# Optimization experiments

Hardware: AMD Instinct MI355X
Metric: run time of the kernel (lower is better)

Reference implementation:

```python
import jax, jax.numpy as jnp
import numpy as np

B, NL, C, H, W = 4, 2048, 128, 128, 128
N_PTS0, N_PTS1 = 32, 8
SCALE = N_PTS0 // N_PTS1  # MaxPool1d kernel/stride
FEATURE_DIM = 5
BN_EPS = 1e-5


def setup_inputs() -> dict:
    key = jax.random.key(0)
    ks = jax.random.split(key, 12)
    fm = jax.random.normal(ks[0], (B, C, H, W), dtype=jnp.float32)
    lines = jax.random.uniform(ks[1], (B, NL, 2, 2), dtype=jnp.float32) * 128.0
    P = C // 2
    s = 0.05
    return {
        "feature_map": fm,
        "lines": lines,
        # Bottleneck1D params (BatchNorm in eval mode: running_mean=0, running_var=1)
        "bn1_g": jnp.ones((C,), jnp.float32), "bn1_b": jnp.zeros((C,), jnp.float32),
        "conv1_w": jax.random.normal(ks[2], (P, C, 1), jnp.float32) * s,
        "conv1_b": jnp.zeros((P,), jnp.float32),
        "bn2_g": jnp.ones((P,), jnp.float32), "bn2_b": jnp.zeros((P,), jnp.float32),
        "conv2_w": jax.random.normal(ks[3], (P, P, 3), jnp.float32) * s,
        "conv2_b": jnp.zeros((P,), jnp.float32),
        "bn3_g": jnp.ones((P,), jnp.float32), "bn3_b": jnp.zeros((P,), jnp.float32),
        "conv3_w": jax.random.normal(ks[4], (C, P, 1), jnp.float32) * s,
        "conv3_b": jnp.zeros((C,), jnp.float32),
        # fc2: ReLU -> Linear(dim_loi*n_pts1 + 5, 4)
        "fc2_w": jax.random.normal(ks[5], (4, C * N_PTS1 + FEATURE_DIM), jnp.float32) * s,
        "fc2_b": jnp.zeros((4,), jnp.float32),
    }


def _bn(x, g, b):
    # eval-mode BatchNorm1d with running_mean=0, running_var=1
    return x * (g / jnp.sqrt(1.0 + BN_EPS))[None, :, None] + b[None, :, None]


def _conv1d(x, w, b, pad):
    y = jax.lax.conv_general_dilated(x, w, (1,), [(pad, pad)],
                                     dimension_numbers=("NCH", "OIH", "NCH"))
    return y + b[None, :, None]


def _loi_gather(fm, lines):
    # sample points along each line: [B, NL, N_PTS0, 2]
    lam = jnp.linspace(0.0, 1.0, N_PTS0, dtype=jnp.float32)[None, None, :, None]
    p = lines[:, :, 0:1, :] * lam + lines[:, :, 1:2, :] * (1.0 - lam) - 0.5
    p = p.reshape(B, -1, 2)                      # [B, NL*N_PTS0, 2]
    px, py = p[..., 0], p[..., 1]
    px0 = jnp.clip(jnp.floor(px), 0.0, 127.0)
    py0 = jnp.clip(jnp.floor(py), 0.0, 127.0)
    px1 = jnp.clip(px0 + 1.0, 0.0, 127.0)
    py1 = jnp.clip(py0 + 1.0, 0.0, 127.0)
    px0l, py0l = px0.astype(jnp.int32), py0.astype(jnp.int32)
    px1l, py1l = px1.astype(jnp.int32), py1.astype(jnp.int32)

    gather = jax.vmap(lambda f, yi, xi: f[:, yi, xi])  # [C, P] per image
    # weights exactly as in the torch source
    xp = (gather(fm, py0l, px0l) * ((px1 - px) * (py1 - py))[:, None, :]
          + gather(fm, py1l, px0l) * ((px - px0) * (py1 - py))[:, None, :]
          + gather(fm, py0l, px1l) * ((px1 - px) * (py - py0))[:, None, :]
          + gather(fm, py1l, px1l) * ((px - px0) * (py - py0))[:, None, :])
    # [B, C, NL*N_PTS0] -> [B*NL, C, N_PTS0]
    xp = xp.reshape(B, C, NL, N_PTS0).transpose(0, 2, 1, 3).reshape(B * NL, C, N_PTS0)
    return xp


def reference(feature_map, lines, bn1_g, bn1_b, conv1_w, conv1_b,
              bn2_g, bn2_b, conv2_w, conv2_b, bn3_g, bn3_b,
              conv3_w, conv3_b, fc2_w, fc2_b):
    xp = _loi_gather(feature_map, lines)               # [B*NL, C, N_PTS0]
    # MaxPool1d(SCALE, SCALE)
    x = xp.reshape(B * NL, C, N_PTS1, SCALE).max(axis=-1)
    # Bottleneck1D residual block
    y = jax.nn.relu(_bn(x, bn1_g, bn1_b))
    y = _conv1d(y, conv1_w, conv1_b, 0)
    y = jax.nn.relu(_bn(y, bn2_g, bn2_b))
    y = _conv1d(y, conv2_w, conv2_b, 1)
    y = jax.nn.relu(_bn(y, bn3_g, bn3_b))
    y = _conv1d(y, conv3_w, conv3_b, 0)
    x = x + y                                          # [B*NL, C, N_PTS1]
    # line geometry feature (use_cood=1, use_slop=1)
    xyu, xyv = lines[:, :, 0, :], lines[:, :, 1, :]
    u2v = jnp.sqrt(((xyu - xyv) ** 2).sum(-1, keepdims=True)).clip(min=1e-6)
    f = jnp.concatenate([xyu / 128.0, xyv / 128.0, u2v], axis=-1)
    f = f.reshape(B * NL, FEATURE_DIM)
    # concat + fc2 (ReLU -> Linear)
    x = jnp.concatenate([x.reshape(B * NL, C * N_PTS1), f], axis=1)
    logits = jax.nn.relu(x) @ fc2_w.T + fc2_b
    prob = jax.nn.softmax(logits, axis=1)
    return logits, prob
```

## Files before the change

kernel.cpp:

```cpp
#include <hip/hip_runtime.h>
#include <math.h>

#define BB 4
#define NLL 2048
#define CC 128
#define HH 128
#define WW 128
#define NPTS0 32
#define NPTS1 8
#define PP 64
#define FDIM 5
#define FCK (CC*NPTS1 + FDIM)
#define FCKP 1032

typedef __attribute__((ext_vector_type(8))) short bf16x8;
typedef __attribute__((ext_vector_type(4))) float f32x4;
typedef __attribute__((ext_vector_type(2))) float f32x2;
typedef __attribute__((ext_vector_type(4))) unsigned u32x4;

__device__ __forceinline__ unsigned short f2bf(float f) {
    union { float f; unsigned u; } v; v.f = f;
    unsigned u = v.u;
    return (unsigned short)((u + 0x7fffu + ((u >> 16) & 1u)) >> 16);
}
__device__ __forceinline__ float bf2f(unsigned short s) {
    union { unsigned u; float f; } v; v.u = ((unsigned)s) << 16;
    return v.f;
}
__device__ __forceinline__ unsigned cvt_pk_bf16(float a, float b) {
    unsigned r;
    asm("v_cvt_pk_bf16_f32 %0, %1, %2" : "=v"(r) : "v"(a), "v"(b));
    return r;
}
__device__ __forceinline__ f32x2 pk_mul(f32x2 a, f32x2 b) {
    f32x2 d;
    asm("v_pk_mul_f32 %0, %1, %2" : "=v"(d) : "v"(a), "v"(b));
    return d;
}
__device__ __forceinline__ f32x2 pk_fma(f32x2 a, f32x2 b, f32x2 c) {
    f32x2 d;
    asm("v_pk_fma_f32 %0, %1, %2, %3" : "=v"(d) : "v"(a), "v"(b), "v"(c));
    return d;
}
__device__ __forceinline__ f32x2 bfpair(unsigned u) {
    union { unsigned v; float f; } lo, hi;
    lo.v = u << 16;
    hi.v = u & 0xffff0000u;
    f32x2 r; r.x = lo.f; r.y = hi.f;
    return r;
}

__global__ __launch_bounds__(256)
void transpose_prep(const float* __restrict__ fm, const float* __restrict__ w1,
                    const float* __restrict__ w2, const float* __restrict__ w3,
                    const float* __restrict__ fcw,
                    unsigned short* __restrict__ fmT,
                    unsigned short* __restrict__ W1b,
                    unsigned short* __restrict__ W2b,
                    unsigned short* __restrict__ W3b,
                    float* __restrict__ fcwP) {
    const int t = threadIdx.x;
    if (blockIdx.x >= 2048) {
        int gid = (blockIdx.x - 2048) * 256 + t;
        for (int e = gid; e < 32800; e += 4096) {
            if (e < 8192) {
                W1b[e] = f2bf(w1[e]);
            } else if (e < 20480) {
                int g = e - 8192;
                int tt = g >> 12, r = g & 4095;
                int p = r >> 6, q = r & 63;
                W2b[tt * 4096 + p * 64 + q] = f2bf(w2[p * 192 + q * 3 + tt]);
            } else if (e < 28672) {
                int g = e - 20480;
                W3b[g] = f2bf(w3[g]);
            } else {
                int g = e - 28672;
                int o = g / FCKP, r = g - o * FCKP;
                fcwP[g] = (r < FCK) ? fcw[o * FCK + r] : 0.0f;
            }
        }
        return;
    }
    __shared__ unsigned short tile[64 * 72];
    const int bh = blockIdx.x;
    const int by = bh >> 2;
    const int xh = (bh >> 1) & 1;
    const int ch = bh & 1;
    const int b = by >> 7, y = by & 127;
    const float* src = fm + ((size_t)b * CC + ch * 64) * (HH * WW)
                     + (size_t)y * WW + xh * 64;
    const int x4 = (t & 15) * 4;
    #pragma unroll
    for (int i = 0; i < 4; ++i) {
        int r = (t >> 4) + 16 * i;
        float4 v = *(const float4*)&src[(size_t)r * (HH * WW) + x4];
        uint2 u;
        u.x = cvt_pk_bf16(v.x, v.y);
        u.y = cvt_pk_bf16(v.z, v.w);
        *(uint2*)&tile[r * 72 + (x4 ^ (r & 28))] = u;
    }
    __syncthreads();
    const int c4 = (t & 15) * 4;
    unsigned short* dst = fmT + ((size_t)by * WW + xh * 64) * CC + ch * 64;
    #pragma unroll
    for (int i = 0; i < 4; ++i) {
        int x = (t >> 4) + 16 * i;
        ushort4 u;
        u.x = tile[(c4 + 0) * 72 + (x ^ ((c4 + 0) & 28))];
        u.y = tile[(c4 + 1) * 72 + (x ^ ((c4 + 1) & 28))];
        u.z = tile[(c4 + 2) * 72 + (x ^ ((c4 + 2) & 28))];
        u.w = tile[(c4 + 3) * 72 + (x ^ ((c4 + 3) & 28))];
        *(ushort4*)&dst[(size_t)x * CC + c4] = u;
    }
}

__global__ __launch_bounds__(256, 5)
void line_mfma(const unsigned short* __restrict__ fmT,
               const float* __restrict__ lines,
               const float* __restrict__ bn1_g, const float* __restrict__ bn1_b,
               const unsigned short* __restrict__ W1b, const float* __restrict__ b1,
               const float* __restrict__ bn2_g, const float* __restrict__ bn2_b,
               const unsigned short* __restrict__ W2b, const float* __restrict__ b2,
               const float* __restrict__ bn3_g, const float* __restrict__ bn3_b,
               const unsigned short* __restrict__ W3b, const float* __restrict__ b3,
               const float* __restrict__ fcwP,  const float* __restrict__ fcb,
               float* __restrict__ out) {
    __shared__ int   s_oA[64], s_oB[64], s_oC[64], s_oD[64];
    __shared__ float s_wA[64], s_wB[64], s_wC[64], s_wD[64];
    __shared__ float s_xs[16 * 132];
    __shared__ unsigned short s_ybn[16 * 136];
    __shared__ unsigned short s_z1[2 * 10 * 72];
    __shared__ unsigned short s_z2[16 * 72];
    __shared__ float s_feat[2][8];
    __shared__ float s_red[4 * 8];

    const int bx  = blockIdx.x;
    const int wg  = (bx & 7) * 512 + (bx >> 3);
    const int L0  = wg * 2;
    const int b   = wg >> 10;
    const int tid = threadIdx.x;
    const int lane = tid & 63;
    const int wv   = tid >> 6;
    const int quad = lane >> 4;
    const int l16  = lane & 15;
    const float inv_s = 1.0f / sqrtf(1.0f + 1e-5f);

    if (tid < 64) {
        int line = tid >> 5, pt = tid & 31;
        const float* ln = lines + (size_t)(L0 + line) * 4;
        float lam = (float)pt * (1.0f / 31.0f);
        float om  = 1.0f - lam;
        float px = ln[0] * lam + ln[2] * om - 0.5f;
        float py = ln[1] * lam + ln[3] * om - 0.5f;
        float px0 = fminf(fmaxf(floorf(px), 0.0f), 127.0f);
        float py0 = fminf(fmaxf(floorf(py), 0.0f), 127.0f);
        float px1 = fminf(px0 + 1.0f, 127.0f);
        float py1 = fminf(py0 + 1.0f, 127.0f);
        int ix0 = (int)px0, ix1 = (int)px1, iy0 = (int)py0, iy1 = (int)py1;
        s_oA[tid] = (iy0 * WW + ix0) * CC;
        s_oB[tid] = (iy1 * WW + ix0) * CC;
        s_oC[tid] = (iy0 * WW + ix1) * CC;
        s_oD[tid] = (iy1 * WW + ix1) * CC;
        float ax = px1 - px, bxv = px - px0, ay = py1 - py, byv = py - py0;
        s_wA[tid] = ax  * ay;
        s_wB[tid] = bxv * ay;
        s_wC[tid] = ax  * byv;
        s_wD[tid] = bxv * byv;
    }
    if (tid >= 64 && tid < 66) {
        int line = tid - 64;
        const float* ln = lines + (size_t)(L0 + line) * 4;
        float ux = ln[0], uy = ln[1], vx = ln[2], vy = ln[3];
        float dx = ux - vx, dy = uy - vy;
        float d = fmaxf(sqrtf(dx * dx + dy * dy), 1e-6f);
        s_feat[line][0] = ux * (1.0f / 128.0f);
        s_feat[line][1] = uy * (1.0f / 128.0f);
        s_feat[line][2] = vx * (1.0f / 128.0f);
        s_feat[line][3] = vy * (1.0f / 128.0f);
        s_feat[line][4] = d;
    }
    if (tid < 128) {
        int line = tid >> 6, q = tid & 63;
        s_z1[line * 720 + 0 * 72 + q] = 0;
        s_z1[line * 720 + 9 * 72 + q] = 0;
    }
    __syncthreads();

    {
        int tl = tid >> 4;
        int c8 = (tid & 15) * 8;
        const unsigned short* base = fmT + (size_t)b * (HH * WW * CC) + c8;
        const int pt0 = (tl >> 3) * 32 + (tl & 7) * 4;
        u32x4 rA[4], rB[4], rC[4], rD[4];
        #pragma unroll
        for (int j = 0; j < 4; ++j) {
            rA[j] = *(const u32x4*)(base + s_oA[pt0 + j]);
            rB[j] = *(const u32x4*)(base + s_oB[pt0 + j]);
            rC[j] = *(const u32x4*)(base + s_oC[pt0 + j]);
            rD[j] = *(const u32x4*)(base + s_oD[pt0 + j]);
        }
        float acc[8];
        #pragma unroll
        for (int i = 0; i < 8; ++i) acc[i] = -INFINITY;
        #pragma unroll
        for (int j = 0; j < 4; ++j) {
            int pt = pt0 + j;
            float wA = s_wA[pt], wB = s_wB[pt], wC = s_wC[pt], wD = s_wD[pt];
            f32x2 wA2 = {wA, wA}, wB2 = {wB, wB};
            f32x2 wC2 = {wC, wC}, wD2 = {wD, wD};
            #pragma unroll
            for (int p2 = 0; p2 < 4; ++p2) {
                f32x2 t = pk_mul(wA2, bfpair(rA[j][p2]));
                t = pk_fma(wB2, bfpair(rB[j][p2]), t);
                t = pk_fma(wC2, bfpair(rC[j][p2]), t);
                t = pk_fma(wD2, bfpair(rD[j][p2]), t);
                acc[2 * p2]     = fmaxf(acc[2 * p2],     t.x);
                acc[2 * p2 + 1] = fmaxf(acc[2 * p2 + 1], t.y);
            }
        }
        float* xr = &s_xs[tl * 132 + c8];
        f32x4 lo = {acc[0], acc[1], acc[2], acc[3]};
        f32x4 hi = {acc[4], acc[5], acc[6], acc[7]};
        *(f32x4*)&xr[0] = lo;
        *(f32x4*)&xr[4] = hi;
        float4 g0 = *(const float4*)(bn1_g + c8);
        float4 g1 = *(const float4*)(bn1_g + c8 + 4);
        float4 v0 = *(const float4*)(bn1_b + c8);
        float4 v1 = *(const float4*)(bn1_b + c8 + 4);
        float y0 = fmaxf(acc[0] * (g0.x * inv_s) + v0.x, 0.0f);
        float y1 = fmaxf(acc[1] * (g0.y * inv_s) + v0.y, 0.0f);
        float y2 = fmaxf(acc[2] * (g0.z * inv_s) + v0.z, 0.0f);
        float y3 = fmaxf(acc[3] * (g0.w * inv_s) + v0.w, 0.0f);
        float y4 = fmaxf(acc[4] * (g1.x * inv_s) + v1.x, 0.0f);
        float y5 = fmaxf(acc[5] * (g1.y * inv_s) + v1.y, 0.0f);
        float y6 = fmaxf(acc[6] * (g1.z * inv_s) + v1.z, 0.0f);
        float y7 = fmaxf(acc[7] * (g1.w * inv_s) + v1.w, 0.0f);
        u32x4 pk;
        pk[0] = cvt_pk_bf16(y0, y1);
        pk[1] = cvt_pk_bf16(y2, y3);
        pk[2] = cvt_pk_bf16(y4, y5);
        pk[3] = cvt_pk_bf16(y6, y7);
        *(u32x4*)&s_ybn[tl * 136 + c8] = pk;
    }
    __syncthreads();

    {
        int n0 = wv * 16;
        f32x4 acc = {0.f, 0.f, 0.f, 0.f};
        #pragma unroll
        for (int kc = 0; kc < 4; ++kc) {
            bf16x8 a = *(const bf16x8*)&s_ybn[l16 * 136 + kc * 32 + quad * 8];
            bf16x8 bf = *(const bf16x8*)(W1b + (n0 + l16) * 128 + kc * 32 + quad * 8);
            acc = __builtin_amdgcn_mfma_f32_16x16x32_bf16(a, bf, acc, 0, 0, 0);
        }
        int p = n0 + l16;
        float s2 = bn2_g[p] * inv_s, bb2 = bn2_b[p], cb = b1[p];
        int line = quad >> 1;
        int kbase = (quad & 1) * 4;
        float v0 = fmaxf((acc[0] + cb) * s2 + bb2, 0.0f);
        float v1 = fmaxf((acc[1] + cb) * s2 + bb2, 0.0f);
        float v2 = fmaxf((acc[2] + cb) * s2 + bb2, 0.0f);
        float v3 = fmaxf((acc[3] + cb) * s2 + bb2, 0.0f);
        unsigned pk01 = cvt_pk_bf16(v0, v1);
        unsigned pk23 = cvt_pk_bf16(v2, v3);
        unsigned short* zr = &s_z1[line * 720 + (kbase + 1) * 72 + p];
        zr[0 * 72] = (unsigned short)pk01;
        zr[1 * 72] = (unsigned short)(pk01 >> 16);
        zr[2 * 72] = (unsigned short)pk23;
        zr[3 * 72] = (unsigned short)(pk23 >> 16);
    }
    __syncthreads();

    {
        int n0 = wv * 16;
        f32x4 acc = {0.f, 0.f, 0.f, 0.f};
        int line = l16 >> 3, k = l16 & 7;
        #pragma unroll
        for (int t = 0; t < 3; ++t) {
            const unsigned short* arow = &s_z1[line * 720 + (k + t) * 72];
            #pragma unroll
            for (int kc = 0; kc < 2; ++kc) {
                bf16x8 a = *(const bf16x8*)&arow[kc * 32 + quad * 8];
                bf16x8 bf = *(const bf16x8*)(W2b + t * 4096 + (n0 + l16) * 64 + kc * 32 + quad * 8);
                acc = __builtin_amdgcn_mfma_f32_16x16x32_bf16(a, bf, acc, 0, 0, 0);
            }
        }
        int p = n0 + l16;
        float s3 = bn3_g[p] * inv_s, bb3 = bn3_b[p], cb = b2[p];
        float v0 = fmaxf((acc[0] + cb) * s3 + bb3, 0.0f);
        float v1 = fmaxf((acc[1] + cb) * s3 + bb3, 0.0f);
        float v2 = fmaxf((acc[2] + cb) * s3 + bb3, 0.0f);
        float v3 = fmaxf((acc[3] + cb) * s3 + bb3, 0.0f);
        unsigned pk01 = cvt_pk_bf16(v0, v1);
        unsigned pk23 = cvt_pk_bf16(v2, v3);
        unsigned short* zr = &s_z2[(quad * 4) * 72 + p];
        zr[0 * 72] = (unsigned short)pk01;
        zr[1 * 72] = (unsigned short)(pk01 >> 16);
        zr[2 * 72] = (unsigned short)pk23;
        zr[3 * 72] = (unsigned short)(pk23 >> 16);
    }
    __syncthreads();

    f32x2 P0 = {0.f, 0.f}, P1v = {0.f, 0.f}, P2v = {0.f, 0.f}, P3v = {0.f, 0.f};
    {
        int kbase = (quad & 1) * 4;
        bf16x8 a0 = *(const bf16x8*)&s_z2[l16 * 72 + 0 * 32 + quad * 8];
        bf16x8 a1 = *(const bf16x8*)&s_z2[l16 * 72 + 1 * 32 + quad * 8];
        #pragma unroll
        for (int sub = 0; sub < 2; ++sub) {
            int n0 = wv * 32 + sub * 16;
            f32x4 acc = {0.f, 0.f, 0.f, 0.f};
            bf16x8 bf0 = *(const bf16x8*)(W3b + (n0 + l16) * 64 + 0 * 32 + quad * 8);
            bf16x8 bf1 = *(const bf16x8*)(W3b + (n0 + l16) * 64 + 1 * 32 + quad * 8);
            acc = __builtin_amdgcn_mfma_f32_16x16x32_bf16(a0, bf0, acc, 0, 0, 0);
            acc = __builtin_amdgcn_mfma_f32_16x16x32_bf16(a1, bf1, acc, 0, 0, 0);
            int c = n0 + l16;
            float cb = b3[c];
            int idx = c * 8 + kbase;
            float4 w0 = *(const float4*)(fcwP + 0 * FCKP + idx);
            float4 w1w = *(const float4*)(fcwP + 1 * FCKP + idx);
            float4 w2w = *(const float4*)(fcwP + 2 * FCKP + idx);
            float4 w3w = *(const float4*)(fcwP + 3 * FCKP + idx);
            #pragma unroll
            for (int rp = 0; rp < 2; ++rp) {
                int m = quad * 4 + rp * 2;
                float e0 = fmaxf(s_xs[m * 132 + c] + acc[rp * 2] + cb, 0.0f);
                float e1 = fmaxf(s_xs[(m + 1) * 132 + c] + acc[rp * 2 + 1] + cb, 0.0f);
                f32x2 vv = {e0, e1};
                float w0lo = rp ? w0.z : w0.x,  w0hi = rp ? w0.w : w0.y;
                float w1lo = rp ? w1w.z : w1w.x, w1hi = rp ? w1w.w : w1w.y;
                float w2lo = rp ? w2w.z : w2w.x, w2hi = rp ? w2w.w : w2w.y;
                float w3lo = rp ? w3w.z : w3w.x, w3hi = rp ? w3w.w : w3w.y;
                f32x2 w0p = {w0lo, w0hi}, w1p = {w1lo, w1hi};
                f32x2 w2p = {w2lo, w2hi}, w3p = {w3lo, w3hi};
                P0  = pk_fma(vv, w0p, P0);
                P1v = pk_fma(vv, w1p, P1v);
                P2v = pk_fma(vv, w2p, P2v);
                P3v = pk_fma(vv, w3p, P3v);
            }
        }
    }
    float p0 = P0.x + P0.y, p1 = P1v.x + P1v.y;
    float p2 = P2v.x + P2v.y, p3 = P3v.x + P3v.y;
    #pragma unroll
    for (int off = 16; off >= 1; off >>= 1) {
        p0 += __shfl_down(p0, off);
        p1 += __shfl_down(p1, off);
        p2 += __shfl_down(p2, off);
        p3 += __shfl_down(p3, off);
    }
    if ((lane & 31) == 0) {
        int line = lane >> 5;
        s_red[wv * 8 + line * 4 + 0] = p0;
        s_red[wv * 8 + line * 4 + 1] = p1;
        s_red[wv * 8 + line * 4 + 2] = p2;
        s_red[wv * 8 + line * 4 + 3] = p3;
    }
    __syncthreads();

    if (tid < 2) {
        int line = tid;
        float lg[4];
        #pragma unroll
        for (int o = 0; o < 4; ++o) {
            lg[o] = fcb[o] + s_red[0 + line * 4 + o] + s_red[8 + line * 4 + o]
                  + s_red[16 + line * 4 + o] + s_red[24 + line * 4 + o];
        }
        #pragma unroll
        for (int j = 0; j < FDIM; ++j) {
            float fv = fmaxf(s_feat[line][j], 0.0f);
            #pragma unroll
            for (int o = 0; o < 4; ++o)
                lg[o] = fmaf(fv, fcwP[o * FCKP + 1024 + j], lg[o]);
        }
        float m = fmaxf(fmaxf(lg[0], lg[1]), fmaxf(lg[2], lg[3]));
        float e0 = expf(lg[0] - m), e1 = expf(lg[1] - m);
        float e2 = expf(lg[2] - m), e3 = expf(lg[3] - m);
        float inv = 1.0f / (e0 + e1 + e2 + e3);
        float* lo = out + (size_t)(L0 + line) * 4;
        lo[0] = lg[0]; lo[1] = lg[1]; lo[2] = lg[2]; lo[3] = lg[3];
        float* pr = out + (size_t)BB * NLL * 4 + (size_t)(L0 + line) * 4;
        pr[0] = e0 * inv; pr[1] = e1 * inv; pr[2] = e2 * inv; pr[3] = e3 * inv;
    }
}

__global__ __launch_bounds__(256)
void transpose_fm2(const float* __restrict__ fm, float* __restrict__ fmT) {
    __shared__ float tile[32 * 132];
    const int c0 = blockIdx.x * 32;
    const int by = blockIdx.y;
    const int b = by >> 7, y = by & 127;
    const int t = threadIdx.x;
    const float* src = fm + ((size_t)b * CC) * (HH * WW) + (size_t)y * WW;
    const int x4 = (t & 31) * 4;
    #pragma unroll
    for (int i = 0; i < 4; ++i) {
        int r = (t >> 5) + 8 * i;
        *(float4*)&tile[r * 132 + x4] =
            *(const float4*)&src[(size_t)(c0 + r) * (HH * WW) + x4];
    }
    __syncthreads();
    float* dst = fmT + (size_t)by * WW * CC + c0 + (t & 31);
    const int cr = (t & 31) * 132;
    #pragma unroll
    for (int i = 0; i < 16; ++i) {
        int x = (t >> 5) + 8 * i;
        dst[(size_t)x * CC] = tile[cr + x];
    }
}

template<bool TRANS>
__global__ __launch_bounds__(256)
void line_kernel_v1(const float* __restrict__ fm,
                    const float* __restrict__ lines,
                    const float* __restrict__ bn1_g, const float* __restrict__ bn1_b,
                    const float* __restrict__ w1,    const float* __restrict__ b1,
                    const float* __restrict__ bn2_g, const float* __restrict__ bn2_b,
                    const float* __restrict__ w2,    const float* __restrict__ b2,
                    const float* __restrict__ bn3_g, const float* __restrict__ bn3_b,
                    const float* __restrict__ w3,    const float* __restrict__ b3,
                    const float* __restrict__ fcw,   const float* __restrict__ fcb,
                    float* __restrict__ out) {
    __shared__ int   s_ix0[32], s_ix1[32], s_iy0[32], s_iy1[32];
    __shared__ float s_wA[32], s_wB[32], s_wC[32], s_wD[32];
    __shared__ float xs [8][132];
    __shared__ float ybn[8][132];
    __shared__ float z1 [64][12];
    __shared__ float z2 [64][8];
    __shared__ float s_feat[8];
    __shared__ float s_red[16];

    const int L   = blockIdx.x;
    const int b   = L / NLL;
    const int tid = threadIdx.x;
    const float inv_s = 1.0f / sqrtf(1.0f + 1e-5f);
    const float* ln = lines + (size_t)L * 4;

    if (tid < 32) {
        float lam = (float)tid * (1.0f / 31.0f);
        float om  = 1.0f - lam;
        float px = ln[0] * lam + ln[2] * om - 0.5f;
        float py = ln[1] * lam + ln[3] * om - 0.5f;
        float px0 = fminf(fmaxf(floorf(px), 0.0f), 127.0f);
        float py0 = fminf(fmaxf(floorf(py), 0.0f), 127.0f);
        float px1 = fminf(px0 + 1.0f, 127.0f);
        float py1 = fminf(py0 + 1.0f, 127.0f);
        s_ix0[tid] = (int)px0; s_ix1[tid] = (int)px1;
        s_iy0[tid] = (int)py0; s_iy1[tid] = (int)py1;
        float ax = px1 - px, bxv = px - px0, ay = py1 - py, byv = py - py0;
        s_wA[tid] = ax  * ay;  s_wB[tid] = bxv * ay;
        s_wC[tid] = ax  * byv; s_wD[tid] = bxv * byv;
    }
    if (tid == 0) {
        float ux = ln[0], uy = ln[1], vx = ln[2], vy = ln[3];
        float dx = ux - vx, dy = uy - vy;
        float d = fmaxf(sqrtf(dx * dx + dy * dy), 1e-6f);
        s_feat[0] = ux / 128.0f; s_feat[1] = uy / 128.0f;
        s_feat[2] = vx / 128.0f; s_feat[3] = vy / 128.0f;
        s_feat[4] = d;
    }
    __syncthreads();
    {
        int cq = tid & 31, k = tid >> 5, c0 = cq * 4;
        float4 acc;
        acc.x = -INFINITY; acc.y = -INFINITY; acc.z = -INFINITY; acc.w = -INFINITY;
        #pragma unroll
        for (int j = 0; j < 4; ++j) {
            int pt = k * 4 + j;
            int ix0 = s_ix0[pt], ix1 = s_ix1[pt];
            int iy0 = s_iy0[pt], iy1 = s_iy1[pt];
            float wA = s_wA[pt], wB = s_wB[pt], wC = s_wC[pt], wD = s_wD[pt];
            float4 vA, vB, vC, vD;
            if (TRANS) {
                const float* base = fm + (size_t)b * HH * WW * CC;
                vA = *(const float4*)(base + ((size_t)(iy0 * WW + ix0)) * CC + c0);
                vB = *(const float4*)(base + ((size_t)(iy1 * WW + ix0)) * CC + c0);
                vC = *(const float4*)(base + ((size_t)(iy0 * WW + ix1)) * CC + c0);
                vD = *(const float4*)(base + ((size_t)(iy1 * WW + ix1)) * CC + c0);
            } else {
                const float* base = fm + ((size_t)b * CC + c0) * HH * WW;
                int oA = iy0 * WW + ix0, oB = iy1 * WW + ix0;
                int oC = iy0 * WW + ix1, oD = iy1 * WW + ix1;
                vA.x = base[oA];           vB.x = base[oB];
                vC.x = base[oC];           vD.x = base[oD];
                vA.y = base[HH*WW + oA];   vB.y = base[HH*WW + oB];
                vC.y = base[HH*WW + oC];   vD.y = base[HH*WW + oD];
                vA.z = base[2*HH*WW + oA]; vB.z = base[2*HH*WW + oB];
                vC.z = base[2*HH*WW + oC]; vD.z = base[2*HH*WW + oD];
                vA.w = base[3*HH*WW + oA]; vB.w = base[3*HH*WW + oB];
                vC.w = base[3*HH*WW + oC]; vD.w = base[3*HH*WW + oD];
            }
            float4 v;
            v.x = wA * vA.x + wB * vB.x + wC * vC.x + wD * vD.x;
            v.y = wA * vA.y + wB * vB.y + wC * vC.y + wD * vD.y;
            v.z = wA * vA.z + wB * vB.z + wC * vC.z + wD * vD.z;
            v.w = wA * vA.w + wB * vB.w + wC * vC.w + wD * vD.w;
            acc.x = fmaxf(acc.x, v.x); acc.y = fmaxf(acc.y, v.y);
            acc.z = fmaxf(acc.z, v.z); acc.w = fmaxf(acc.w, v.w);
        }
        *(float4*)(&xs[k][c0]) = acc;
    }
    __syncthreads();
    for (int e = tid; e < 1024; e += 256) {
        int k = e >> 7, c = e & 127;
        ybn[k][c] = fmaxf(xs[k][c] * (bn1_g[c] * inv_s) + bn1_b[c], 0.0f);
    }
    __syncthreads();
    if (tid < 64) { z1[tid][0] = 0.0f; z1[tid][9] = 0.0f; }
    {
        int p = tid >> 2, kq = tid & 3;
        const float* wrow = w1 + p * 128;
        float a0a = 0.f, a0b = 0.f, a1a = 0.f, a1b = 0.f;
        #pragma unroll 8
        for (int c = 0; c < 128; c += 4) {
            float4 w  = *(const float4*)(wrow + c);
            float4 ya = *(const float4*)(&ybn[kq][c]);
            float4 yb = *(const float4*)(&ybn[kq + 4][c]);
            a0a = fmaf(w.x, ya.x, a0a); a0b = fmaf(w.y, ya.y, a0b);
            a0a = fmaf(w.z, ya.z, a0a); a0b = fmaf(w.w, ya.w, a0b);
            a1a = fmaf(w.x, yb.x, a1a); a1b = fmaf(w.y, yb.y, a1b);
            a1a = fmaf(w.z, yb.z, a1a); a1b = fmaf(w.w, yb.w, a1b);
        }
        float s2 = bn2_g[p] * inv_s, bb = bn2_b[p], cb = b1[p];
        z1[p][1 + kq]     = fmaxf((a0a + a0b + cb) * s2 + bb, 0.0f);
        z1[p][1 + kq + 4] = fmaxf((a1a + a1b + cb) * s2 + bb, 0.0f);
    }
    __syncthreads();
    {
        int p = tid >> 2, kq = tid & 3;
        const float* wrow = w2 + p * 192;
        float acc0 = 0.f, acc1 = 0.f;
        #pragma unroll 4
        for (int q = 0; q < 64; ++q) {
            float w0 = wrow[q * 3 + 0], w1v = wrow[q * 3 + 1], w2v = wrow[q * 3 + 2];
            const float* zr = &z1[q][0];
            acc0 = fmaf(w0, zr[kq], acc0);
            acc0 = fmaf(w1v, zr[kq + 1], acc0);
            acc0 = fmaf(w2v, zr[kq + 2], acc0);
            acc1 = fmaf(w0, zr[kq + 4], acc1);
            acc1 = fmaf(w1v, zr[kq + 5], acc1);
            acc1 = fmaf(w2v, zr[kq + 6], acc1);
        }
        float s3 = bn3_g[p] * inv_s, bb = bn3_b[p], cb = b2[p];
        z2[p][kq]     = fmaxf((acc0 + cb) * s3 + bb, 0.0f);
        z2[p][kq + 4] = fmaxf((acc1 + cb) * s3 + bb, 0.0f);
    }
    __syncthreads();
    float part0 = 0.f, part1 = 0.f, part2 = 0.f, part3 = 0.f;
    {
        int c = tid >> 1, kq = tid & 1;
        const float* wrow = w3 + c * 64;
        float acc[4] = {0.f, 0.f, 0.f, 0.f};
        #pragma unroll 8
        for (int q = 0; q < 64; ++q) {
            float w = wrow[q];
            acc[0] = fmaf(w, z2[q][kq], acc[0]);
            acc[1] = fmaf(w, z2[q][kq + 2], acc[1]);
            acc[2] = fmaf(w, z2[q][kq + 4], acc[2]);
            acc[3] = fmaf(w, z2[q][kq + 6], acc[3]);
        }
        float cb = b3[c];
        #pragma unroll
        for (int i = 0; i < 4; ++i) {
            int k = kq + 2 * i;
            float v = fmaxf(xs[k][c] + acc[i] + cb, 0.0f);
            int idx = c * 8 + k;
            part0 = fmaf(v, fcw[0 * FCK + idx], part0);
            part1 = fmaf(v, fcw[1 * FCK + idx], part1);
            part2 = fmaf(v, fcw[2 * FCK + idx], part2);
            part3 = fmaf(v, fcw[3 * FCK + idx], part3);
        }
    }
    #pragma unroll
    for (int off = 32; off > 0; off >>= 1) {
        part0 += __shfl_down(part0, off);
        part1 += __shfl_down(part1, off);
        part2 += __shfl_down(part2, off);
        part3 += __shfl_down(part3, off);
    }
    if ((tid & 63) == 0) {
        int w = tid >> 6;
        s_red[w * 4 + 0] = part0; s_red[w * 4 + 1] = part1;
        s_red[w * 4 + 2] = part2; s_red[w * 4 + 3] = part3;
    }
    __syncthreads();
    if (tid == 0) {
        float lg[4];
        #pragma unroll
        for (int o = 0; o < 4; ++o)
            lg[o] = fcb[o] + s_red[o] + s_red[4 + o] + s_red[8 + o] + s_red[12 + o];
        #pragma unroll
        for (int j = 0; j < FDIM; ++j) {
            float fv = fmaxf(s_feat[j], 0.0f);
            #pragma unroll
            for (int o = 0; o < 4; ++o)
                lg[o] = fmaf(fv, fcw[o * FCK + 1024 + j], lg[o]);
        }
        float m = fmaxf(fmaxf(lg[0], lg[1]), fmaxf(lg[2], lg[3]));
        float e0 = expf(lg[0] - m), e1 = expf(lg[1] - m);
        float e2 = expf(lg[2] - m), e3 = expf(lg[3] - m);
        float inv = 1.0f / (e0 + e1 + e2 + e3);
        float* lo = out + (size_t)L * 4;
        lo[0] = lg[0]; lo[1] = lg[1]; lo[2] = lg[2]; lo[3] = lg[3];
        float* pr = out + (size_t)BB * NLL * 4 + (size_t)L * 4;
        pr[0] = e0 * inv; pr[1] = e1 * inv; pr[2] = e2 * inv; pr[3] = e3 * inv;
    }
}

extern "C" void kernel_launch(void* const* d_in, const int* in_sizes, int n_in,
                              void* d_out, int out_size, void* d_ws, size_t ws_size,
                              hipStream_t stream) {
    const float* fm     = (const float*)d_in[0];
    const float* lines  = (const float*)d_in[1];
    const float* bn1_g  = (const float*)d_in[2];
    const float* bn1_b  = (const float*)d_in[3];
    const float* w1     = (const float*)d_in[4];
    const float* b1     = (const float*)d_in[5];
    const float* bn2_g  = (const float*)d_in[6];
    const float* bn2_b  = (const float*)d_in[7];
    const float* w2     = (const float*)d_in[8];
    const float* b2     = (const float*)d_in[9];
    const float* bn3_g  = (const float*)d_in[10];
    const float* bn3_b  = (const float*)d_in[11];
    const float* w3     = (const float*)d_in[12];
    const float* b3     = (const float*)d_in[13];
    const float* fcw    = (const float*)d_in[14];
    const float* fcb    = (const float*)d_in[15];
    float* out = (float*)d_out;

    const size_t fmTb_bytes = (size_t)BB * HH * WW * CC * sizeof(unsigned short);
    const size_t fmTf_bytes = (size_t)BB * HH * WW * CC * sizeof(float);
    const size_t wb_bytes   = 57344;
    const size_t fcwP_bytes = 4 * FCKP * sizeof(float);

    if (ws_size >= fmTb_bytes + wb_bytes + fcwP_bytes) {
        unsigned short* fmT = (unsigned short*)d_ws;
        unsigned short* W1b = (unsigned short*)((char*)d_ws + fmTb_bytes);
        unsigned short* W2b = W1b + 8192;
        unsigned short* W3b = W2b + 12288;
        float* fcwP = (float*)((char*)d_ws + fmTb_bytes + wb_bytes);
        transpose_prep<<<2048 + 16, 256, 0, stream>>>(
            fm, w1, w2, w3, fcw, fmT, W1b, W2b, W3b, fcwP);
        line_mfma<<<BB * NLL / 2, 256, 0, stream>>>(
            fmT, lines, bn1_g, bn1_b, W1b, b1, bn2_g, bn2_b, W2b, b2,
            bn3_g, bn3_b, W3b, b3, fcwP, fcb, out);
    } else if (ws_size >= fmTf_bytes) {
        float* fmT = (float*)d_ws;
        dim3 tg(CC / 32, BB * HH);
        transpose_fm2<<<tg, 256, 0, stream>>>(fm, fmT);
        line_kernel_v1<true><<<BB * NLL, 256, 0, stream>>>(
            fmT, lines, bn1_g, bn1_b, w1, b1, bn2_g, bn2_b, w2, b2,
            bn3_g, bn3_b, w3, b3, fcw, fcb, out);
    } else {
        line_kernel_v1<false><<<BB * NLL, 256, 0, stream>>>(
            fm, lines, bn1_g, bn1_b, w1, b1, bn2_g, bn2_b, w2, b2,
            bn3_g, bn3_b, w3, b3, fcw, fcb, out);
    }
}
```

Measured before the change: 150.5 us.

## Process two line pairs per block and prefetch the second gather during the conv chain

Each block now handles four lines as two pairs instead of two lines. The bilinear gather loads for the second pair are issued before the first pair's MFMA conv chain and consumed afterwards, hiding global-gather latency behind compute. __syncthreads is replaced with an LDS-only waitcnt plus s_barrier so in-flight global loads are not drained at barriers. The cost is more live VGPRs, with the launch-bounds occupancy hint lowered from 5 to 4, and half as many blocks.

```diff
diff --git a/kernel.cpp b/kernel.cpp
--- a/kernel.cpp
+++ b/kernel.cpp
@@ -48,6 +48,10 @@
     hi.v = u & 0xffff0000u;
     f32x2 r; r.x = lo.f; r.y = hi.f;
     return r;
+}
+__device__ __forceinline__ void bar_lds() {
+    asm volatile("s_waitcnt lgkmcnt(0)" ::: "memory");
+    __builtin_amdgcn_s_barrier();
 }
 
 __global__ __launch_bounds__(256)
@@ -114,7 +118,7 @@
     }
 }
 
-__global__ __launch_bounds__(256, 5)
+__global__ __launch_bounds__(256, 4)
 void line_mfma(const unsigned short* __restrict__ fmT,
                const float* __restrict__ lines,
                const float* __restrict__ bn1_g, const float* __restrict__ bn1_b,
@@ -125,19 +129,19 @@
                const unsigned short* __restrict__ W3b, const float* __restrict__ b3,
                const float* __restrict__ fcwP,  const float* __restrict__ fcb,
                float* __restrict__ out) {
-    __shared__ int   s_oA[64], s_oB[64], s_oC[64], s_oD[64];
-    __shared__ float s_wA[64], s_wB[64], s_wC[64], s_wD[64];
+    __shared__ int   s_oA[128], s_oB[128], s_oC[128], s_oD[128];
+    __shared__ float s_wA[128], s_wB[128], s_wC[128], s_wD[128];
     __shared__ float s_xs[16 * 132];
     __shared__ unsigned short s_ybn[16 * 136];
     __shared__ unsigned short s_z1[2 * 10 * 72];
     __shared__ unsigned short s_z2[16 * 72];
-    __shared__ float s_feat[2][8];
+    __shared__ float s_feat[4][8];
     __shared__ float s_red[4 * 8];
 
     const int bx  = blockIdx.x;
-    const int wg  = (bx & 7) * 512 + (bx >> 3);
-    const int L0  = wg * 2;
-    const int b   = wg >> 10;
+    const int wg  = (bx & 7) * 256 + (bx >> 3);
+    const int L0  = wg * 4;
+    const int b   = wg >> 9;
     const int tid = threadIdx.x;
     const int lane = tid & 63;
     const int wv   = tid >> 6;
@@ -145,7 +149,7 @@
     const int l16  = lane & 15;
     const float inv_s = 1.0f / sqrtf(1.0f + 1e-5f);
 
-    if (tid < 64) {
+    if (tid < 128) {
         int line = tid >> 5, pt = tid & 31;
         const float* ln = lines + (size_t)(L0 + line) * 4;
         float lam = (float)pt * (1.0f / 31.0f);
@@ -167,8 +171,8 @@
         s_wC[tid] = ax  * byv;
         s_wD[tid] = bxv * byv;
     }
-    if (tid >= 64 && tid < 66) {
-        int line = tid - 64;
+    if (tid >= 128 && tid < 132) {
+        int line = tid - 128;
         const float* ln = lines + (size_t)(L0 + line) * 4;
         float ux = ln[0], uy = ln[1], vx = ln[2], vy = ln[3];
         float dx = ux - vx, dy = uy - vy;
@@ -179,32 +183,44 @@
         s_feat[line][3] = vy * (1.0f / 128.0f);
         s_feat[line][4] = d;
     }
-    if (tid < 128) {
-        int line = tid >> 6, q = tid & 63;
+    if (tid >= 132 && tid < 260 && tid - 132 < 128) {
+        int e = tid - 132;
+        int line = e >> 6, q = e & 63;
         s_z1[line * 720 + 0 * 72 + q] = 0;
         s_z1[line * 720 + 9 * 72 + q] = 0;
     }
-    __syncthreads();
-
-    {
-        int tl = tid >> 4;
-        int c8 = (tid & 15) * 8;
-        const unsigned short* base = fmT + (size_t)b * (HH * WW * CC) + c8;
-        const int pt0 = (tl >> 3) * 32 + (tl & 7) * 4;
-        u32x4 rA[4], rB[4], rC[4], rD[4];
+    if (tid < 4) {
+        int e = 124 + tid;
+        int line = e >> 6, q = e & 63;
+        s_z1[line * 720 + 0 * 72 + q] = 0;
+        s_z1[line * 720 + 9 * 72 + q] = 0;
+    }
+    bar_lds();
+
+    const int tl = tid >> 4;
+    const int c8 = (tid & 15) * 8;
+    const unsigned short* gbase = fmT + (size_t)b * (HH * WW * CC) + c8;
+
+    auto gather_issue = [&](int pair, u32x4* rA, u32x4* rB, u32x4* rC, u32x4* rD) {
+        int ptb = (pair * 2 + (tl >> 3)) * 32 + (tl & 7) * 4;
         #pragma unroll
         for (int j = 0; j < 4; ++j) {
-            rA[j] = *(const u32x4*)(base + s_oA[pt0 + j]);
-            rB[j] = *(const u32x4*)(base + s_oB[pt0 + j]);
-            rC[j] = *(const u32x4*)(base + s_oC[pt0 + j]);
-            rD[j] = *(const u32x4*)(base + s_oD[pt0 + j]);
-        }
+            rA[j] = *(const u32x4*)(gbase + s_oA[ptb + j]);
+            rB[j] = *(const u32x4*)(gbase + s_oB[ptb + j]);
+            rC[j] = *(const u32x4*)(gbase + s_oC[ptb + j]);
+            rD[j] = *(const u32x4*)(gbase + s_oD[ptb + j]);
+        }
+    };
+
+    auto bilinear = [&](int pair, const u32x4* rA, const u32x4* rB,
+                        const u32x4* rC, const u32x4* rD) {
+        int ptb = (pair * 2 + (tl >> 3)) * 32 + (tl & 7) * 4;
         float acc[8];
         #pragma unroll
         for (int i = 0; i < 8; ++i) acc[i] = -INFINITY;
         #pragma unroll
         for (int j = 0; j < 4; ++j) {
-            int pt = pt0 + j;
+            int pt = ptb + j;
             float wA = s_wA[pt], wB = s_wB[pt], wC = s_wC[pt], wD = s_wD[pt];
             f32x2 wA2 = {wA, wA}, wB2 = {wB, wB};
             f32x2 wC2 = {wC, wC}, wD2 = {wD, wD};
@@ -241,147 +257,168 @@
         pk[2] = cvt_pk_bf16(y4, y5);
         pk[3] = cvt_pk_bf16(y6, y7);
         *(u32x4*)&s_ybn[tl * 136 + c8] = pk;
-    }
-    __syncthreads();
+    };
+
+    auto conv_chain = [&]() {
+        {
+            int n0 = wv * 16;
+            f32x4 acc = {0.f, 0.f, 0.f, 0.f};
+            #pragma unroll
+            for (int kc = 0; kc < 4; ++kc) {
+                bf16x8 a = *(const bf16x8*)&s_ybn[l16 * 136 + kc * 32 + quad * 8];
+                bf16x8 bf = *(const bf16x8*)(W1b + (n0 + l16) * 128 + kc * 32 + quad * 8);
+                acc = __builtin_amdgcn_mfma_f32_16x16x32_bf16(a, bf, acc, 0, 0, 0);
+            }
+            int p = n0 + l16;
+            float s2 = bn2_g[p] * inv_s, bb2 = bn2_b[p], cb = b1[p];
+            int line = quad >> 1;
+            int kbase = (quad & 1) * 4;
+            float v0 = fmaxf((acc[0] + cb) * s2 + bb2, 0.0f);
+            float v1 = fmaxf((acc[1] + cb) * s2 + bb2, 0.0f);
+            float v2 = fmaxf((acc[2] + cb) * s2 + bb2, 0.0f);
+            float v3 = fmaxf((acc[3] + cb) * s2 + bb2, 0.0f);
+            unsigned pk01 = cvt_pk_bf16(v0, v1);
+            unsigned pk23 = cvt_pk_bf16(v2, v3);
+            unsigned short* zr = &s_z1[line * 720 + (kbase + 1) * 72 + p];
+            zr[0 * 72] = (unsigned short)pk01;
+            zr[1 * 72] = (unsigned short)(pk01 >> 16);
+            zr[2 * 72] = (unsigned short)pk23;
+            zr[3 * 72] = (unsigned short)(pk23 >> 16);
+        }
+        bar_lds();
+        {
+            int n0 = wv * 16;
+            f32x4 acc = {0.f, 0.f, 0.f, 0.f};
+            int line = l16 >> 3, k = l16 & 7;
+            #pragma unroll
+            for (int t = 0; t < 3; ++t) {
+                const unsigned short* arow = &s_z1[line * 720 + (k + t) * 72];
+                #pragma unroll
+                for (int kc = 0; kc < 2; ++kc) {
+                    bf16x8 a = *(const bf16x8*)&arow[kc * 32 + quad * 8];
+                    bf16x8 bf = *(const bf16x8*)(W2b + t * 4096 + (n0 + l16) * 64 + kc * 32 + quad * 8);
+                    acc = __builtin_amdgcn_mfma_f32_16x16x32_bf16(a, bf, acc, 0, 0, 0);
+                }
+            }
+            int p = n0 + l16;
+            float s3 = bn3_g[p] * inv_s, bb3 = bn3_b[p], cb = b2[p];
+            float v0 = fmaxf((acc[0] + cb) * s3 + bb3, 0.0f);
+            float v1 = fmaxf((acc[1] + cb) * s3 + bb3, 0.0f);
+            float v2 = fmaxf((acc[2] + cb) * s3 + bb3, 0.0f);
+            float v3 = fmaxf((acc[3] + cb) * s3 + bb3, 0.0f);
+            unsigned pk01 = cvt_pk_bf16(v0, v1);
+            unsigned pk23 = cvt_pk_bf16(v2, v3);
+            unsigned short* zr = &s_z2[(quad * 4) * 72 + p];
+            zr[0 * 72] = (unsigned short)pk01;
+            zr[1 * 72] = (unsigned short)(pk01 >> 16);
+            zr[2 * 72] = (unsigned short)pk23;
+            zr[3 * 72] = (unsigned short)(pk23 >> 16);
+        }
+        bar_lds();
+        f32x2 P0 = {0.f, 0.f}, P1v = {0.f, 0.f}, P2v = {0.f, 0.f}, P3v = {0.f, 0.f};
+        {
+            int kbase = (quad & 1) * 4;
+            bf16x8 a0 = *(const bf16x8*)&s_z2[l16 * 72 + 0 * 32 + quad * 8];
+            bf16x8 a1 = *(const bf16x8*)&s_z2[l16 * 72 + 1 * 32 + quad * 8];
+            #pragma unroll
+            for (int sub = 0; sub < 2; ++sub) {
+                int n0 = wv * 32 + sub * 16;
+                f32x4 acc = {0.f, 0.f, 0.f, 0.f};
+                bf16x8 bf0 = *(const bf16x8*)(W3b + (n0 + l16) * 64 + 0 * 32 + quad * 8);
+                bf16x8 bf1 = *(const bf16x8*)(W3b + (n0 + l16) * 64 + 1 * 32 + quad * 8);
+                acc = __builtin_amdgcn_mfma_f32_16x16x32_bf16(a0, bf0, acc, 0, 0, 0);
+                acc = __builtin_amdgcn_mfma_f32_16x16x32_bf16(a1, bf1, acc, 0, 0, 0);
+                int c = n0 + l16;
+                float cb = b3[c];
+                int idx = c * 8 + kbase;
+                float4 w0 = *(const float4*)(fcwP + 0 * FCKP + idx);
+                float4 w1w = *(const float4*)(fcwP + 1 * FCKP + idx);
+                float4 w2w = *(const float4*)(fcwP + 2 * FCKP + idx);
+                float4 w3w = *(const float4*)(fcwP + 3 * FCKP + idx);
+                #pragma unroll
+                for (int rp = 0; rp < 2; ++rp) {
+                    int m = quad * 4 + rp * 2;
+                    float e0 = fmaxf(s_xs[m * 132 + c] + acc[rp * 2] + cb, 0.0f);
+                    float e1 = fmaxf(s_xs[(m + 1) * 132 + c] + acc[rp * 2 + 1] + cb, 0.0f);
+                    f32x2 vv = {e0, e1};
+                    float w0lo = rp ? w0.z : w0.x,  w0hi = rp ? w0.w : w0.y;
+                    float w1lo = rp ? w1w.z : w1w.x, w1hi = rp ? w1w.w : w1w.y;
+                    float w2lo = rp ? w2w.z : w2w.x, w2hi = rp ? w2w.w : w2w.y;
+                    float w3lo = rp ? w3w.z : w3w.x, w3hi = rp ? w3w.w : w3w.y;
+                    f32x2 w0p = {w0lo, w0hi}, w1p = {w1lo, w1hi};
+                    f32x2 w2p = {w2lo, w2hi}, w3p = {w3lo, w3hi};
+                    P0  = pk_fma(vv, w0p, P0);
+                    P1v = pk_fma(vv, w1p, P1v);
+                    P2v = pk_fma(vv, w2p, P2v);
+                    P3v = pk_fma(vv, w3p, P3v);
+                }
+            }
+        }
+        float p0 = P0.x + P0.y, p1 = P1v.x + P1v.y;
+        float p2 = P2v.x + P2v.y, p3 = P3v.x + P3v.y;
+        #pragma unroll
+        for (int off = 16; off >= 1; off >>= 1) {
+            p0 += __shfl_down(p0, off);
+            p1 += __shfl_down(p1, off);
+            p2 += __shfl_down(p2, off);
+            p3 += __shfl_down(p3, off);
+        }
+        if ((lane & 31) == 0) {
+            int line = lane >> 5;
+            s_red[wv * 8 + line * 4 + 0] = p0;
+            s_red[wv * 8 + line * 4 + 1] = p1;
+            s_red[wv * 8 + line * 4 + 2] = p2;
+            s_red[wv * 8 + line * 4 + 3] = p3;
+        }
+        bar_lds();
+    };
+
+    auto finish = [&](int pair) {
+        if (tid < 2) {
+            int line = tid;
+            float lg[4];
+            #pragma unroll
+            for (int o = 0; o < 4; ++o) {
+                lg[o] = fcb[o] + s_red[0 + line * 4 + o] + s_red[8 + line * 4 + o]
+                      + s_red[16 + line * 4 + o] + s_red[24 + line * 4 + o];
+            }
+            #pragma unroll
+            for (int j = 0; j < FDIM; ++j) {
+                float fv = fmaxf(s_feat[pair * 2 + line][j], 0.0f);
+                #pragma unroll
+                for (int o = 0; o < 4; ++o)
+                    lg[o] = fmaf(fv, fcwP[o * FCKP + 1024 + j], lg[o]);
+            }
+            float m = fmaxf(fmaxf(lg[0], lg[1]), fmaxf(lg[2], lg[3]));
+            float e0 = expf(lg[0] - m), e1 = expf(lg[1] - m);
+            float e2 = expf(lg[2] - m), e3 = expf(lg[3] - m);
+            float inv = 1.0f / (e0 + e1 + e2 + e3);
+            size_t Lg = (size_t)(L0 + pair * 2 + line);
+            float* lo = out + Lg * 4;
+            lo[0] = lg[0]; lo[1] = lg[1]; lo[2] = lg[2]; lo[3] = lg[3];
+            float* pr = out + (size_t)BB * NLL * 4 + Lg * 4;
+            pr[0] = e0 * inv; pr[1] = e1 * inv; pr[2] = e2 * inv; pr[3] = e3 * inv;
+        }
+    };
 
     {
-        int n0 = wv * 16;
-        f32x4 acc = {0.f, 0.f, 0.f, 0.f};
-        #pragma unroll
-        for (int kc = 0; kc < 4; ++kc) {
-            bf16x8 a = *(const bf16x8*)&s_ybn[l16 * 136 + kc * 32 + quad * 8];
-            bf16x8 bf = *(const bf16x8*)(W1b + (n0 + l16) * 128 + kc * 32 + quad * 8);
-            acc = __builtin_amdgcn_mfma_f32_16x16x32_bf16(a, bf, acc, 0, 0, 0);
-        }
-        int p = n0 + l16;
-        float s2 = bn2_g[p] * inv_s, bb2 = bn2_b[p], cb = b1[p];
-        int line = quad >> 1;
-        int kbase = (quad & 1) * 4;
-        float v0 = fmaxf((acc[0] + cb) * s2 + bb2, 0.0f);
-        float v1 = fmaxf((acc[1] + cb) * s2 + bb2, 0.0f);
-        float v2 = fmaxf((acc[2] + cb) * s2 + bb2, 0.0f);
-        float v3 = fmaxf((acc[3] + cb) * s2 + bb2, 0.0f);
-        unsigned pk01 = cvt_pk_bf16(v0, v1);
-        unsigned pk23 = cvt_pk_bf16(v2, v3);
-        unsigned short* zr = &s_z1[line * 720 + (kbase + 1) * 72 + p];
-        zr[0 * 72] = (unsigned short)pk01;
-        zr[1 * 72] = (unsigned short)(pk01 >> 16);
-        zr[2 * 72] = (unsigned short)pk23;
-        zr[3 * 72] = (unsigned short)(pk23 >> 16);
-    }
-    __syncthreads();
-
-    {
-        int n0 = wv * 16;
-        f32x4 acc = {0.f, 0.f, 0.f, 0.f};
-        int line = l16 >> 3, k = l16 & 7;
-        #pragma unroll
-        for (int t = 0; t < 3; ++t) {
-            const unsigned short* arow = &s_z1[line * 720 + (k + t) * 72];
-            #pragma unroll
-            for (int kc = 0; kc < 2; ++kc) {
-                bf16x8 a = *(const bf16x8*)&arow[kc * 32 + quad * 8];
-                bf16x8 bf = *(const bf16x8*)(W2b + t * 4096 + (n0 + l16) * 64 + kc * 32 + quad * 8);
-                acc = __builtin_amdgcn_mfma_f32_16x16x32_bf16(a, bf, acc, 0, 0, 0);
-            }
-        }
-        int p = n0 + l16;
-        float s3 = bn3_g[p] * inv_s, bb3 = bn3_b[p], cb = b2[p];
-        float v0 = fmaxf((acc[0] + cb) * s3 + bb3, 0.0f);
-        float v1 = fmaxf((acc[1] + cb) * s3 + bb3, 0.0f);
-        float v2 = fmaxf((acc[2] + cb) * s3 + bb3, 0.0f);
-        float v3 = fmaxf((acc[3] + cb) * s3 + bb3, 0.0f);
-        unsigned pk01 = cvt_pk_bf16(v0, v1);
-        unsigned pk23 = cvt_pk_bf16(v2, v3);
-        unsigned short* zr = &s_z2[(quad * 4) * 72 + p];
-        zr[0 * 72] = (unsigned short)pk01;
-        zr[1 * 72] = (unsigned short)(pk01 >> 16);
-        zr[2 * 72] = (unsigned short)pk23;
-        zr[3 * 72] = (unsigned short)(pk23 >> 16);
-    }
-    __syncthreads();
-
-    f32x2 P0 = {0.f, 0.f}, P1v = {0.f, 0.f}, P2v = {0.f, 0.f}, P3v = {0.f, 0.f};
-    {
-        int kbase = (quad & 1) * 4;
-        bf16x8 a0 = *(const bf16x8*)&s_z2[l16 * 72 + 0 * 32 + quad * 8];
-        bf16x8 a1 = *(const bf16x8*)&s_z2[l16 * 72 + 1 * 32 + quad * 8];
-        #pragma unroll
-        for (int sub = 0; sub < 2; ++sub) {
-            int n0 = wv * 32 + sub * 16;
-            f32x4 acc = {0.f, 0.f, 0.f, 0.f};
-            bf16x8 bf0 = *(const bf16x8*)(W3b + (n0 + l16) * 64 + 0 * 32 + quad * 8);
-            bf16x8 bf1 = *(const bf16x8*)(W3b + (n0 + l16) * 64 + 1 * 32 + quad * 8);
-            acc = __builtin_amdgcn_mfma_f32_16x16x32_bf16(a0, bf0, acc, 0, 0, 0);
-            acc = __builtin_amdgcn_mfma_f32_16x16x32_bf16(a1, bf1, acc, 0, 0, 0);
-            int c = n0 + l16;
-            float cb = b3[c];
-            int idx = c * 8 + kbase;
-            float4 w0 = *(const float4*)(fcwP + 0 * FCKP + idx);
-            float4 w1w = *(const float4*)(fcwP + 1 * FCKP + idx);
-            float4 w2w = *(const float4*)(fcwP + 2 * FCKP + idx);
-            float4 w3w = *(const float4*)(fcwP + 3 * FCKP + idx);
-            #pragma unroll
-            for (int rp = 0; rp < 2; ++rp) {
-                int m = quad * 4 + rp * 2;
-                float e0 = fmaxf(s_xs[m * 132 + c] + acc[rp * 2] + cb, 0.0f);
-                float e1 = fmaxf(s_xs[(m + 1) * 132 + c] + acc[rp * 2 + 1] + cb, 0.0f);
-                f32x2 vv = {e0, e1};
-                float w0lo = rp ? w0.z : w0.x,  w0hi = rp ? w0.w : w0.y;
-                float w1lo = rp ? w1w.z : w1w.x, w1hi = rp ? w1w.w : w1w.y;
-                float w2lo = rp ? w2w.z : w2w.x, w2hi = rp ? w2w.w : w2w.y;
-                float w3lo = rp ? w3w.z : w3w.x, w3hi = rp ? w3w.w : w3w.y;
-                f32x2 w0p = {w0lo, w0hi}, w1p = {w1lo, w1hi};
-                f32x2 w2p = {w2lo, w2hi}, w3p = {w3lo, w3hi};
-                P0  = pk_fma(vv, w0p, P0);
-                P1v = pk_fma(vv, w1p, P1v);
-                P2v = pk_fma(vv, w2p, P2v);
-                P3v = pk_fma(vv, w3p, P3v);
-            }
-        }
-    }
-    float p0 = P0.x + P0.y, p1 = P1v.x + P1v.y;
-    float p2 = P2v.x + P2v.y, p3 = P3v.x + P3v.y;
-    #pragma unroll
-    for (int off = 16; off >= 1; off >>= 1) {
-        p0 += __shfl_down(p0, off);
-        p1 += __shfl_down(p1, off);
-        p2 += __shfl_down(p2, off);
-        p3 += __shfl_down(p3, off);
-    }
-    if ((lane & 31) == 0) {
-        int line = lane >> 5;
-        s_red[wv * 8 + line * 4 + 0] = p0;
-        s_red[wv * 8 + line * 4 + 1] = p1;
-        s_red[wv * 8 + line * 4 + 2] = p2;
-        s_red[wv * 8 + line * 4 + 3] = p3;
-    }
-    __syncthreads();
-
-    if (tid < 2) {
-        int line = tid;
-        float lg[4];
-        #pragma unroll
-        for (int o = 0; o < 4; ++o) {
-            lg[o] = fcb[o] + s_red[0 + line * 4 + o] + s_red[8 + line * 4 + o]
-                  + s_red[16 + line * 4 + o] + s_red[24 + line * 4 + o];
-        }
-        #pragma unroll
-        for (int j = 0; j < FDIM; ++j) {
-            float fv = fmaxf(s_feat[line][j], 0.0f);
-            #pragma unroll
-            for (int o = 0; o < 4; ++o)
-                lg[o] = fmaf(fv, fcwP[o * FCKP + 1024 + j], lg[o]);
-        }
-        float m = fmaxf(fmaxf(lg[0], lg[1]), fmaxf(lg[2], lg[3]));
-        float e0 = expf(lg[0] - m), e1 = expf(lg[1] - m);
-        float e2 = expf(lg[2] - m), e3 = expf(lg[3] - m);
-        float inv = 1.0f / (e0 + e1 + e2 + e3);
-        float* lo = out + (size_t)(L0 + line) * 4;
-        lo[0] = lg[0]; lo[1] = lg[1]; lo[2] = lg[2]; lo[3] = lg[3];
-        float* pr = out + (size_t)BB * NLL * 4 + (size_t)(L0 + line) * 4;
-        pr[0] = e0 * inv; pr[1] = e1 * inv; pr[2] = e2 * inv; pr[3] = e3 * inv;
-    }
+        u32x4 rA[4], rB[4], rC[4], rD[4];
+        gather_issue(0, rA, rB, rC, rD);
+        bilinear(0, rA, rB, rC, rD);
+    }
+    u32x4 nA[4], nB[4], nC[4], nD[4];
+    gather_issue(1, nA, nB, nC, nD);
+    __builtin_amdgcn_sched_barrier(0);
+    bar_lds();
+
+    conv_chain();
+
+    finish(0);
+    bilinear(1, nA, nB, nC, nD);
+    bar_lds();
+
+    conv_chain();
+    finish(1);
 }
 
 __global__ __launch_bounds__(256)
@@ -641,7 +678,7 @@
         float* fcwP = (float*)((char*)d_ws + fmTb_bytes + wb_bytes);
         transpose_prep<<<2048 + 16, 256, 0, stream>>>(
             fm, w1, w2, w3, fcw, fmT, W1b, W2b, W3b, fcwP);
-        line_mfma<<<BB * NLL / 2, 256, 0, stream>>>(
+        line_mfma<<<BB * NLL / 4, 256, 0, stream>>>(
             fmT, lines, bn1_g, bn1_b, W1b, b1, bn2_g, bn2_b, W2b, b2,
             bn3_g, bn3_b, W3b, b3, fcwP, fcb, out);
     } else if (ws_size >= fmTf_bytes) {
```

Result: slower. 169.6 us (+12.7%).
